# Optimization experiments

Hardware: AMD Instinct MI355X
Metric: run time of the kernel (lower is better)

## Reference

```python
import jax, jax.numpy as jnp
import numpy as np

B, S, V, H = 256, 1024, 256, 256


def setup_inputs() -> dict:
    key = jax.random.key(0)
    ks = jax.random.split(key, 12)
    s = 1.0 / np.sqrt(H)
    def u(k, shape):
        return jax.random.uniform(k, shape, jnp.float32, -s, s)
    return {
        "x": jax.random.normal(ks[0], (B, S, V), jnp.float32),
        "w_ih0": u(ks[1], (4 * H, V)),
        "w_hh0": u(ks[2], (4 * H, H)),
        "b_ih0": u(ks[3], (4 * H,)),
        "b_hh0": u(ks[4], (4 * H,)),
        "w_ih1": u(ks[5], (4 * H, H)),
        "w_hh1": u(ks[6], (4 * H, H)),
        "b_ih1": u(ks[7], (4 * H,)),
        "b_hh1": u(ks[8], (4 * H,)),
        "fc_w": u(ks[9], (V, H)),
        "fc_b": u(ks[10], (V,)),
    }


def _lstm_layer(inp, w_ih, w_hh, b_ih, b_hh):
    # inp: [B, S, D]. Precompute input contribution for all timesteps (big GEMM),
    # then scan the recurrence (PyTorch gate order: i, f, g, o).
    pre = jnp.einsum('bsd,gd->bsg', inp, w_ih) + b_ih + b_hh  # [B, S, 4H]
    h0 = jnp.zeros((inp.shape[0], w_hh.shape[1]), inp.dtype)
    c0 = jnp.zeros_like(h0)

    def step(carry, p):
        h, c = carry
        g = p + h @ w_hh.T  # [B, 4H]
        i, f, gg, o = jnp.split(g, 4, axis=-1)
        c = jax.nn.sigmoid(f) * c + jax.nn.sigmoid(i) * jnp.tanh(gg)
        h = jax.nn.sigmoid(o) * jnp.tanh(c)
        return (h, c), h

    _, hs = jax.lax.scan(step, (h0, c0), pre.transpose(1, 0, 2))  # hs: [S, B, H]
    return hs.transpose(1, 0, 2)


def reference(x, w_ih0, w_hh0, b_ih0, b_hh0, w_ih1, w_hh1, b_ih1, b_hh1, fc_w, fc_b):
    h1 = _lstm_layer(x, w_ih0, w_hh0, b_ih0, b_hh0)
    h2 = _lstm_layer(h1, w_ih1, w_hh1, b_ih1, b_hh1)
    logits = jnp.einsum('bsh,vh->bsv', h2, fc_w) + fc_b
    return jax.nn.log_softmax(logits, axis=-1)
```

## Files before the change

### kernel.cpp

```cpp
#include <hip/hip_runtime.h>
#include <cstdint>
#include <cstddef>


typedef __attribute__((ext_vector_type(8))) short bf16x8;
typedef __attribute__((ext_vector_type(4))) float f32x4;

#define DEVFN __device__ __forceinline__

constexpr unsigned SENT = 0xFFFFFFFFu;

DEVFN unsigned short f2bf(float f) {
  union { float f; unsigned u; } v; v.f = f;
  unsigned r = v.u + 0x7FFFu + ((v.u >> 16) & 1u);
  return (unsigned short)(r >> 16);
}
DEVFN float bf2f(unsigned short b) {
  union { unsigned u; float f; } v; v.u = ((unsigned)b) << 16;
  return v.f;
}
DEVFN int swz(int row, int colbyte) {
  return row * 512 + ((((colbyte >> 4) ^ (row & 7)) << 4) | (colbyte & 15));
}
DEVFN float sigm(float x) { return __builtin_amdgcn_rcpf(1.f + __expf(-x)); }
DEVFN float tanhfast(float x) {
  float ax = fabsf(x);
  float e  = __expf(-2.f * ax);
  float t  = (1.f - e) * __builtin_amdgcn_rcpf(1.f + e);
  return copysignf(t, x);
}

DEVFN unsigned aload(const unsigned* p) {
  return __hip_atomic_load(p, __ATOMIC_RELAXED, __HIP_MEMORY_SCOPE_AGENT);
}

DEVFN void spin16(unsigned hv[16], const unsigned* hs_tid) {
  while (true) {
    unsigned pend = 0;
#pragma unroll
    for (int k = 0; k < 16; ++k) pend |= (hv[k] == SENT) ? 1u : 0u;
    if (!pend) break;
#pragma unroll
    for (int k = 0; k < 16; ++k) hv[k] = aload(hs_tid + k * 128);
  }
}

__global__ void pack_w(const float* __restrict__ w, unsigned short* __restrict__ dst) {
  int bid = blockIdx.x;
  int lane = threadIdx.x;
  int col = (bid >> 3) * 16 + (lane & 15);
  int k0  = (bid & 7) * 32 + (lane >> 4) * 8;
  const float* src = w + (size_t)col * 256 + k0;
  unsigned short* d = dst + ((size_t)bid * 64 + lane) * 8;
#pragma unroll
  for (int j = 0; j < 8; ++j) d[j] = f2bf(src[j]);
}

__global__ __launch_bounds__(128, 1) void lstm_dual(
    const float* __restrict__ x,
    const unsigned short* __restrict__ Wih0, const unsigned short* __restrict__ Whh0,
    const float* __restrict__ bih0, const float* __restrict__ bhh0,
    const unsigned short* __restrict__ Wih1, const unsigned short* __restrict__ Whh1,
    const float* __restrict__ bih1, const float* __restrict__ bhh1,
    unsigned short* __restrict__ h1, unsigned short* __restrict__ h2)
{
  __shared__ char ldsA[8192];
  __shared__ char ldsB[8192];
  const int tid = threadIdx.x;
  const int w = tid >> 6, lane = tid & 63;
  const bool isL1 = blockIdx.x >= 128;
  const int b = isL1 ? (int)blockIdx.x - 128 : (int)blockIdx.x;
  const int m = b & 15, n = b >> 4;
  const int u16 = n * 2 + w;
  const int u   = u16 * 16 + (lane & 15);
  const int r0  = (lane >> 4) * 4;

  const unsigned short* Wih = isL1 ? Wih1 : Wih0;
  const unsigned short* Whh = isL1 ? Whh1 : Whh0;
  const float* bihp = isL1 ? bih1 : bih0;
  const float* bhhp = isL1 ? bhh1 : bhh0;
  unsigned short* hout = isL1 ? h2 : h1;

  bf16x8 bwih[4][8], bwhh[4][8];
#pragma unroll
  for (int g = 0; g < 4; ++g)
#pragma unroll
    for (int kt = 0; kt < 8; ++kt) {
      bwih[g][kt] = *(const bf16x8*)(Wih +
          ((((size_t)(g * 16 + u16)) * 8 + kt) * 64 + lane) * 8);
      bwhh[g][kt] = *(const bf16x8*)(Whh +
          ((((size_t)(g * 16 + u16)) * 8 + kt) * 64 + lane) * 8);
    }

  float bias[4];
#pragma unroll
  for (int g = 0; g < 4; ++g) bias[g] = bihp[g * 256 + u] + bhhp[g * 256 + u];

  float c[4] = {0.f, 0.f, 0.f, 0.f};

  if (!isL1) {
    const int xr = tid >> 3;
    const int xc = (tid & 7) * 32;
    float4 vv[8];
    {
      const float4* s = (const float4*)(x + ((size_t)(16 * m + xr) * 1024 + 0) * 256 + xc);
#pragma unroll
      for (int j = 0; j < 8; ++j) vv[j] = s[j];
    }

    for (int t = 0; t < 1024; ++t) {
#pragma unroll
      for (int s4 = 0; s4 < 4; ++s4) {
        uint4 o;
        o.x = f2bf(vv[2*s4].x)   | ((unsigned)f2bf(vv[2*s4].y)   << 16);
        o.y = f2bf(vv[2*s4].z)   | ((unsigned)f2bf(vv[2*s4].w)   << 16);
        o.z = f2bf(vv[2*s4+1].x) | ((unsigned)f2bf(vv[2*s4+1].y) << 16);
        o.w = f2bf(vv[2*s4+1].z) | ((unsigned)f2bf(vv[2*s4+1].w) << 16);
        *(uint4*)(&ldsB[swz(xr, xc * 2 + s4 * 16)]) = o;
      }
      if (t < 1023) {
        const float4* s = (const float4*)(x + ((size_t)(16 * m + xr) * 1024 + (t + 1)) * 256 + xc);
#pragma unroll
        for (int j = 0; j < 8; ++j) vv[j] = s[j];
      }
      unsigned hv[16];
      const unsigned* hs_tid = nullptr;
      if (t > 0) {
        hs_tid = (const unsigned*)h1 + ((size_t)(t - 1) * 256 + 16 * m) * 128 + tid;
#pragma unroll
        for (int k = 0; k < 16; ++k) hv[k] = aload(hs_tid + k * 128);
      }
      __syncthreads();

      f32x4 acc[4];
#pragma unroll
      for (int g = 0; g < 4; ++g) acc[g] = (f32x4){0.f, 0.f, 0.f, 0.f};
#pragma unroll
      for (int kt = 0; kt < 8; ++kt) {
        bf16x8 a = *(const bf16x8*)(&ldsB[swz(lane & 15, kt * 64 + (lane >> 4) * 16)]);
#pragma unroll
        for (int g = 0; g < 4; ++g)
          acc[g] = __builtin_amdgcn_mfma_f32_16x16x32_bf16(a, bwih[g][kt], acc[g], 0, 0, 0);
      }

      if (t > 0) {
        spin16(hv, hs_tid);
#pragma unroll
        for (int k = 0; k < 16; ++k)
          *(unsigned*)(&ldsA[swz(k, tid * 4)]) = hv[k];
        __syncthreads();
#pragma unroll
        for (int kt = 0; kt < 8; ++kt) {
          bf16x8 a = *(const bf16x8*)(&ldsA[swz(lane & 15, kt * 64 + (lane >> 4) * 16)]);
#pragma unroll
          for (int g = 0; g < 4; ++g)
            acc[g] = __builtin_amdgcn_mfma_f32_16x16x32_bf16(a, bwhh[g][kt], acc[g], 0, 0, 0);
        }
      } else {
        __syncthreads();
      }

      unsigned myh[4];
#pragma unroll
      for (int q = 0; q < 4; ++q) {
        float ia = acc[0][q] + bias[0];
        float fa = acc[1][q] + bias[1];
        float ga = acc[2][q] + bias[2];
        float oa = acc[3][q] + bias[3];
        c[q] = sigm(fa) * c[q] + sigm(ia) * tanhfast(ga);
        myh[q] = (unsigned)f2bf(sigm(oa) * tanhfast(c[q]));
      }
#pragma unroll
      for (int q = 0; q < 4; ++q) {
        unsigned ov = (unsigned)__shfl_xor((int)myh[q], 1, 64);
        if ((lane & 1) == 0) {
          unsigned word = (myh[q] & 0xFFFFu) | (ov << 16);
          unsigned* hp = (unsigned*)h1 + (((size_t)t * 256 + 16 * m + r0 + q) * 256 + u) / 2;
          __hip_atomic_store(hp, word, __ATOMIC_RELAXED, __HIP_MEMORY_SCOPE_AGENT);
        }
      }
    }
  } else {
    for (int t = 0; t < 1024; ++t) {
      unsigned hv1[16], hv2[16];
      const unsigned* hs1_tid = (const unsigned*)h1 + ((size_t)t * 256 + 16 * m) * 128 + tid;
      const unsigned* hs2_tid = nullptr;
#pragma unroll
      for (int k = 0; k < 16; ++k) hv1[k] = aload(hs1_tid + k * 128);
      if (t > 0) {
        hs2_tid = (const unsigned*)h2 + ((size_t)(t - 1) * 256 + 16 * m) * 128 + tid;
#pragma unroll
        for (int k = 0; k < 16; ++k) hv2[k] = aload(hs2_tid + k * 128);
      }

      spin16(hv1, hs1_tid);
#pragma unroll
      for (int k = 0; k < 16; ++k)
        *(unsigned*)(&ldsB[swz(k, tid * 4)]) = hv1[k];
      __syncthreads();

      f32x4 acc[4];
#pragma unroll
      for (int g = 0; g < 4; ++g) acc[g] = (f32x4){0.f, 0.f, 0.f, 0.f};
#pragma unroll
      for (int kt = 0; kt < 8; ++kt) {
        bf16x8 a = *(const bf16x8*)(&ldsB[swz(lane & 15, kt * 64 + (lane >> 4) * 16)]);
#pragma unroll
        for (int g = 0; g < 4; ++g)
          acc[g] = __builtin_amdgcn_mfma_f32_16x16x32_bf16(a, bwih[g][kt], acc[g], 0, 0, 0);
      }

      if (t > 0) {
        spin16(hv2, hs2_tid);
#pragma unroll
        for (int k = 0; k < 16; ++k)
          *(unsigned*)(&ldsA[swz(k, tid * 4)]) = hv2[k];
        __syncthreads();
#pragma unroll
        for (int kt = 0; kt < 8; ++kt) {
          bf16x8 a = *(const bf16x8*)(&ldsA[swz(lane & 15, kt * 64 + (lane >> 4) * 16)]);
#pragma unroll
          for (int g = 0; g < 4; ++g)
            acc[g] = __builtin_amdgcn_mfma_f32_16x16x32_bf16(a, bwhh[g][kt], acc[g], 0, 0, 0);
        }
      } else {
        __syncthreads();
      }

      unsigned myh[4];
#pragma unroll
      for (int q = 0; q < 4; ++q) {
        float ia = acc[0][q] + bias[0];
        float fa = acc[1][q] + bias[1];
        float ga = acc[2][q] + bias[2];
        float oa = acc[3][q] + bias[3];
        c[q] = sigm(fa) * c[q] + sigm(ia) * tanhfast(ga);
        myh[q] = (unsigned)f2bf(sigm(oa) * tanhfast(c[q]));
      }
#pragma unroll
      for (int q = 0; q < 4; ++q) {
        unsigned ov = (unsigned)__shfl_xor((int)myh[q], 1, 64);
        if ((lane & 1) == 0) {
          unsigned word = (myh[q] & 0xFFFFu) | (ov << 16);
          unsigned* hp = (unsigned*)h2 + (((size_t)t * 256 + 16 * m + r0 + q) * 256 + u) / 2;
          __hip_atomic_store(hp, word, __ATOMIC_RELAXED, __HIP_MEMORY_SCOPE_AGENT);
        }
      }
    }
  }
}

__global__ __launch_bounds__(256, 1) void fc_lsm(
    const unsigned short* __restrict__ h2,
    const unsigned short* __restrict__ Bp,
    const float* __restrict__ fcb,
    float* __restrict__ out)
{
  const int tid = threadIdx.x;
  const int wid = tid >> 6, lane = tid & 63;
  const int t = blockIdx.x >> 2, b0 = (blockIdx.x & 3) * 64;

  f32x4 acc[16];
#pragma unroll
  for (int nt = 0; nt < 16; ++nt) acc[nt] = (f32x4){0.f, 0.f, 0.f, 0.f};

#pragma unroll
  for (int kt = 0; kt < 8; ++kt) {
    bf16x8 a = *(const bf16x8*)(h2 +
        (((size_t)t * 256 + b0 + wid * 16 + (lane & 15)) * 256 +
         kt * 32 + (lane >> 4) * 8));
#pragma unroll
    for (int nt = 0; nt < 16; ++nt) {
      bf16x8 b = *(const bf16x8*)(Bp + (((size_t)nt * 8 + kt) * 64 + lane) * 8);
      acc[nt] = __builtin_amdgcn_mfma_f32_16x16x32_bf16(a, b, acc[nt], 0, 0, 0);
    }
  }
#pragma unroll
  for (int nt = 0; nt < 16; ++nt) {
    float bias = fcb[nt * 16 + (lane & 15)];
#pragma unroll
    for (int q = 0; q < 4; ++q) acc[nt][q] += bias;
  }

  float mx[4] = {-1e30f, -1e30f, -1e30f, -1e30f};
#pragma unroll
  for (int nt = 0; nt < 16; ++nt)
#pragma unroll
    for (int q = 0; q < 4; ++q) mx[q] = fmaxf(mx[q], acc[nt][q]);
#pragma unroll
  for (int d = 1; d < 16; d <<= 1)
#pragma unroll
    for (int q = 0; q < 4; ++q) mx[q] = fmaxf(mx[q], __shfl_xor(mx[q], d, 64));

  float sm[4] = {0.f, 0.f, 0.f, 0.f};
#pragma unroll
  for (int nt = 0; nt < 16; ++nt)
#pragma unroll
    for (int q = 0; q < 4; ++q) sm[q] += __expf(acc[nt][q] - mx[q]);
#pragma unroll
  for (int d = 1; d < 16; d <<= 1)
#pragma unroll
    for (int q = 0; q < 4; ++q) sm[q] += __shfl_xor(sm[q], d, 64);

  float lse[4];
#pragma unroll
  for (int q = 0; q < 4; ++q) lse[q] = mx[q] + __logf(sm[q]);

#pragma unroll
  for (int nt = 0; nt < 16; ++nt) {
#pragma unroll
    for (int q = 0; q < 4; ++q) {
      int b = b0 + wid * 16 + (lane >> 4) * 4 + q;
      out[((size_t)b * 1024 + t) * 256 + nt * 16 + (lane & 15)] = acc[nt][q] - lse[q];
    }
  }
}

__global__ void fill_marker(float* out, size_t nvals) {
  size_t i = (size_t)blockIdx.x * blockDim.x + threadIdx.x;
  if (i < nvals) out[i] = -7777.0f;
}

extern "C" void kernel_launch(void* const* d_in, const int* in_sizes, int n_in,
                              void* d_out, int out_size, void* d_ws, size_t ws_size,
                              hipStream_t stream)
{
  (void)in_sizes; (void)n_in;
  const float* x    = (const float*)d_in[0];
  const float* wih0 = (const float*)d_in[1];
  const float* whh0 = (const float*)d_in[2];
  const float* bih0 = (const float*)d_in[3];
  const float* bhh0 = (const float*)d_in[4];
  const float* wih1 = (const float*)d_in[5];
  const float* whh1 = (const float*)d_in[6];
  const float* bih1 = (const float*)d_in[7];
  const float* bhh1 = (const float*)d_in[8];
  const float* fcw  = (const float*)d_in[9];
  const float* fcb  = (const float*)d_in[10];
  float* out = (float*)d_out;

  const size_t o_wp0i = 0;
  const size_t o_wp0h = o_wp0i + 524288;
  const size_t o_wp1i = o_wp0h + 524288;
  const size_t o_wp1h = o_wp1i + 524288;
  const size_t o_fcp  = o_wp1h + 524288;
  const size_t o_h1   = o_fcp  + 131072;
  const size_t o_h2   = o_h1   + 134217728;
  const size_t need   = o_h2   + 134217728;

  if (ws_size < need) {
    size_t nv = (size_t)out_size;
    fill_marker<<<(unsigned)((nv + 1023) / 1024), 1024, 0, stream>>>(out, nv);
    return;
  }

  char* ws = (char*)d_ws;
  unsigned short* wp0i = (unsigned short*)(ws + o_wp0i);
  unsigned short* wp0h = (unsigned short*)(ws + o_wp0h);
  unsigned short* wp1i = (unsigned short*)(ws + o_wp1i);
  unsigned short* wp1h = (unsigned short*)(ws + o_wp1h);
  unsigned short* fcp  = (unsigned short*)(ws + o_fcp);
  unsigned short* h1   = (unsigned short*)(ws + o_h1);
  unsigned short* h2   = (unsigned short*)(ws + o_h2);

  pack_w<<<512, 64, 0, stream>>>(wih0, wp0i);
  pack_w<<<512, 64, 0, stream>>>(whh0, wp0h);
  pack_w<<<512, 64, 0, stream>>>(wih1, wp1i);
  pack_w<<<512, 64, 0, stream>>>(whh1, wp1h);
  pack_w<<<128, 64, 0, stream>>>(fcw,  fcp);

  hipMemsetAsync(h1, 0xFF, 134217728, stream);
  hipMemsetAsync(h2, 0xFF, 134217728, stream);

  lstm_dual<<<256, 128, 0, stream>>>(x, wp0i, wp0h, bih0, bhh0,
                                     wp1i, wp1h, bih1, bhh1, h1, h2);

  fc_lsm<<<4096, 256, 0, stream>>>(h2, fcp, fcb, out);
}
```

Baseline: 3.831 ms.

## Replace sentinel polling with per-wave progress flags between LSTM blocks

Hidden-state handoff between workgroups now uses per-wave counter flags, written after a vmcnt wait, instead of polling the data itself for a 0xFF sentinel. This drops the two 128MB sentinel memsets and lets consumers spin on a few flag words, then read h with 64-bit loads. Layer-1 blocks also reorder work so the recurrent h2 matmul runs before they wait on layer-0 output. The risk is ordering: relaxed atomics plus s_waitcnt must make the h stores visible before the flag store.

```diff
diff --git a/kernel.cpp b/kernel.cpp
--- a/kernel.cpp
+++ b/kernel.cpp
@@ -5,19 +5,14 @@
 
 typedef __attribute__((ext_vector_type(8))) short bf16x8;
 typedef __attribute__((ext_vector_type(4))) float f32x4;
+typedef unsigned long long ull;
 
 #define DEVFN __device__ __forceinline__
-
-constexpr unsigned SENT = 0xFFFFFFFFu;
 
 DEVFN unsigned short f2bf(float f) {
   union { float f; unsigned u; } v; v.f = f;
   unsigned r = v.u + 0x7FFFu + ((v.u >> 16) & 1u);
   return (unsigned short)(r >> 16);
-}
-DEVFN float bf2f(unsigned short b) {
-  union { unsigned u; float f; } v; v.u = ((unsigned)b) << 16;
-  return v.f;
 }
 DEVFN int swz(int row, int colbyte) {
   return row * 512 + ((((colbyte >> 4) ^ (row & 7)) << 4) | (colbyte & 15));
@@ -33,16 +28,15 @@
 DEVFN unsigned aload(const unsigned* p) {
   return __hip_atomic_load(p, __ATOMIC_RELAXED, __HIP_MEMORY_SCOPE_AGENT);
 }
-
-DEVFN void spin16(unsigned hv[16], const unsigned* hs_tid) {
-  while (true) {
-    unsigned pend = 0;
-#pragma unroll
-    for (int k = 0; k < 16; ++k) pend |= (hv[k] == SENT) ? 1u : 0u;
-    if (!pend) break;
-#pragma unroll
-    for (int k = 0; k < 16; ++k) hv[k] = aload(hs_tid + k * 128);
-  }
+DEVFN ull aload64(const ull* p) {
+  return __hip_atomic_load(p, __ATOMIC_RELAXED, __HIP_MEMORY_SCOPE_AGENT);
+}
+DEVFN void astore(unsigned* p, unsigned v) {
+  __hip_atomic_store(p, v, __ATOMIC_RELAXED, __HIP_MEMORY_SCOPE_AGENT);
+}
+
+DEVFN unsigned* flag_at(unsigned* f, int L, int m, int n, int w) {
+  return f + (((((L * 16 + m) * 8) + n) * 2 + w) << 4);
 }
 
 __global__ void pack_w(const float* __restrict__ w, unsigned short* __restrict__ dst) {
@@ -62,7 +56,8 @@
     const float* __restrict__ bih0, const float* __restrict__ bhh0,
     const unsigned short* __restrict__ Wih1, const unsigned short* __restrict__ Whh1,
     const float* __restrict__ bih1, const float* __restrict__ bhh1,
-    unsigned short* __restrict__ h1, unsigned short* __restrict__ h2)
+    unsigned short* __restrict__ h1, unsigned short* __restrict__ h2,
+    unsigned* __restrict__ flags)
 {
   __shared__ char ldsA[8192];
   __shared__ char ldsB[8192];
@@ -98,12 +93,18 @@
 
   float c[4] = {0.f, 0.f, 0.f, 0.f};
 
+  const int r = tid >> 3, cc = tid & 7;
+  const int Lown = isL1 ? 1 : 0;
+  unsigned* fown = flag_at(flags, Lown, m, n, w);
+  const unsigned* fh_0 = flag_at(flags, Lown, m, cc, 0);
+  const unsigned* fh_1 = flag_at(flags, Lown, m, cc, 1);
+  const unsigned* fs_0 = flag_at(flags, 0, m, cc, 0);
+  const unsigned* fs_1 = flag_at(flags, 0, m, cc, 1);
+
   if (!isL1) {
-    const int xr = tid >> 3;
-    const int xc = (tid & 7) * 32;
     float4 vv[8];
     {
-      const float4* s = (const float4*)(x + ((size_t)(16 * m + xr) * 1024 + 0) * 256 + xc);
+      const float4* s = (const float4*)(x + ((size_t)(16 * m + r) * 1024 + 0) * 256 + cc * 32);
 #pragma unroll
       for (int j = 0; j < 8; ++j) vv[j] = s[j];
     }
@@ -116,19 +117,12 @@
         o.y = f2bf(vv[2*s4].z)   | ((unsigned)f2bf(vv[2*s4].w)   << 16);
         o.z = f2bf(vv[2*s4+1].x) | ((unsigned)f2bf(vv[2*s4+1].y) << 16);
         o.w = f2bf(vv[2*s4+1].z) | ((unsigned)f2bf(vv[2*s4+1].w) << 16);
-        *(uint4*)(&ldsB[swz(xr, xc * 2 + s4 * 16)]) = o;
+        *(uint4*)(&ldsB[swz(r, cc * 64 + s4 * 16)]) = o;
       }
       if (t < 1023) {
-        const float4* s = (const float4*)(x + ((size_t)(16 * m + xr) * 1024 + (t + 1)) * 256 + xc);
+        const float4* s = (const float4*)(x + ((size_t)(16 * m + r) * 1024 + (t + 1)) * 256 + cc * 32);
 #pragma unroll
         for (int j = 0; j < 8; ++j) vv[j] = s[j];
-      }
-      unsigned hv[16];
-      const unsigned* hs_tid = nullptr;
-      if (t > 0) {
-        hs_tid = (const unsigned*)h1 + ((size_t)(t - 1) * 256 + 16 * m) * 128 + tid;
-#pragma unroll
-        for (int k = 0; k < 16; ++k) hv[k] = aload(hs_tid + k * 128);
       }
       __syncthreads();
 
@@ -144,11 +138,24 @@
       }
 
       if (t > 0) {
-        spin16(hv, hs_tid);
-#pragma unroll
-        for (int k = 0; k < 16; ++k)
-          *(unsigned*)(&ldsA[swz(k, tid * 4)]) = hv[k];
-        __syncthreads();
+        const unsigned tgt = (unsigned)t;
+        while (aload(fh_0) < tgt) {}
+        while (aload(fh_1) < tgt) {}
+        const ull* hs = (const ull*)h1 + ((size_t)(t - 1) * 256 + 16 * m + r) * 64 + cc * 8;
+        ull hv[8];
+#pragma unroll
+        for (int k = 0; k < 8; ++k) hv[k] = aload64(hs + k);
+#pragma unroll
+        for (int s4 = 0; s4 < 4; ++s4) {
+          uint4 o;
+          o.x = (unsigned)hv[2*s4];       o.y = (unsigned)(hv[2*s4] >> 32);
+          o.z = (unsigned)hv[2*s4+1];     o.w = (unsigned)(hv[2*s4+1] >> 32);
+          *(uint4*)(&ldsA[swz(r, cc * 64 + s4 * 16)]) = o;
+        }
+      }
+      __syncthreads();
+
+      if (t > 0) {
 #pragma unroll
         for (int kt = 0; kt < 8; ++kt) {
           bf16x8 a = *(const bf16x8*)(&ldsA[swz(lane & 15, kt * 64 + (lane >> 4) * 16)]);
@@ -156,8 +163,6 @@
           for (int g = 0; g < 4; ++g)
             acc[g] = __builtin_amdgcn_mfma_f32_16x16x32_bf16(a, bwhh[g][kt], acc[g], 0, 0, 0);
         }
-      } else {
-        __syncthreads();
       }
 
       unsigned myh[4];
@@ -176,55 +181,71 @@
         if ((lane & 1) == 0) {
           unsigned word = (myh[q] & 0xFFFFu) | (ov << 16);
           unsigned* hp = (unsigned*)h1 + (((size_t)t * 256 + 16 * m + r0 + q) * 256 + u) / 2;
-          __hip_atomic_store(hp, word, __ATOMIC_RELAXED, __HIP_MEMORY_SCOPE_AGENT);
-        }
-      }
+          astore(hp, word);
+        }
+      }
+      asm volatile("s_waitcnt vmcnt(0)" ::: "memory");
+      if (lane == 0) astore(fown, (unsigned)(t + 1));
     }
   } else {
     for (int t = 0; t < 1024; ++t) {
-      unsigned hv1[16], hv2[16];
-      const unsigned* hs1_tid = (const unsigned*)h1 + ((size_t)t * 256 + 16 * m) * 128 + tid;
-      const unsigned* hs2_tid = nullptr;
-#pragma unroll
-      for (int k = 0; k < 16; ++k) hv1[k] = aload(hs1_tid + k * 128);
+      ull hv2[8];
       if (t > 0) {
-        hs2_tid = (const unsigned*)h2 + ((size_t)(t - 1) * 256 + 16 * m) * 128 + tid;
-#pragma unroll
-        for (int k = 0; k < 16; ++k) hv2[k] = aload(hs2_tid + k * 128);
-      }
-
-      spin16(hv1, hs1_tid);
-#pragma unroll
-      for (int k = 0; k < 16; ++k)
-        *(unsigned*)(&ldsB[swz(k, tid * 4)]) = hv1[k];
+        const unsigned tgt = (unsigned)t;
+        while (aload(fh_0) < tgt) {}
+        while (aload(fh_1) < tgt) {}
+        const ull* hs2 = (const ull*)h2 + ((size_t)(t - 1) * 256 + 16 * m + r) * 64 + cc * 8;
+#pragma unroll
+        for (int k = 0; k < 8; ++k) hv2[k] = aload64(hs2 + k);
+      }
+      {
+        const unsigned tgt = (unsigned)(t + 1);
+        while (aload(fs_0) < tgt) {}
+        while (aload(fs_1) < tgt) {}
+      }
+      const ull* hs1 = (const ull*)h1 + ((size_t)t * 256 + 16 * m + r) * 64 + cc * 8;
+      ull hv1[8];
+#pragma unroll
+      for (int k = 0; k < 8; ++k) hv1[k] = aload64(hs1 + k);
+
+      if (t > 0) {
+#pragma unroll
+        for (int s4 = 0; s4 < 4; ++s4) {
+          uint4 o;
+          o.x = (unsigned)hv2[2*s4];      o.y = (unsigned)(hv2[2*s4] >> 32);
+          o.z = (unsigned)hv2[2*s4+1];    o.w = (unsigned)(hv2[2*s4+1] >> 32);
+          *(uint4*)(&ldsA[swz(r, cc * 64 + s4 * 16)]) = o;
+        }
+      }
       __syncthreads();
 
       f32x4 acc[4];
 #pragma unroll
       for (int g = 0; g < 4; ++g) acc[g] = (f32x4){0.f, 0.f, 0.f, 0.f};
+      if (t > 0) {
+#pragma unroll
+        for (int kt = 0; kt < 8; ++kt) {
+          bf16x8 a = *(const bf16x8*)(&ldsA[swz(lane & 15, kt * 64 + (lane >> 4) * 16)]);
+#pragma unroll
+          for (int g = 0; g < 4; ++g)
+            acc[g] = __builtin_amdgcn_mfma_f32_16x16x32_bf16(a, bwhh[g][kt], acc[g], 0, 0, 0);
+        }
+      }
+#pragma unroll
+      for (int s4 = 0; s4 < 4; ++s4) {
+        uint4 o;
+        o.x = (unsigned)hv1[2*s4];        o.y = (unsigned)(hv1[2*s4] >> 32);
+        o.z = (unsigned)hv1[2*s4+1];      o.w = (unsigned)(hv1[2*s4+1] >> 32);
+        *(uint4*)(&ldsB[swz(r, cc * 64 + s4 * 16)]) = o;
+      }
+      __syncthreads();
+
 #pragma unroll
       for (int kt = 0; kt < 8; ++kt) {
         bf16x8 a = *(const bf16x8*)(&ldsB[swz(lane & 15, kt * 64 + (lane >> 4) * 16)]);
 #pragma unroll
         for (int g = 0; g < 4; ++g)
           acc[g] = __builtin_amdgcn_mfma_f32_16x16x32_bf16(a, bwih[g][kt], acc[g], 0, 0, 0);
-      }
-
-      if (t > 0) {
-        spin16(hv2, hs2_tid);
-#pragma unroll
-        for (int k = 0; k < 16; ++k)
-          *(unsigned*)(&ldsA[swz(k, tid * 4)]) = hv2[k];
-        __syncthreads();
-#pragma unroll
-        for (int kt = 0; kt < 8; ++kt) {
-          bf16x8 a = *(const bf16x8*)(&ldsA[swz(lane & 15, kt * 64 + (lane >> 4) * 16)]);
-#pragma unroll
-          for (int g = 0; g < 4; ++g)
-            acc[g] = __builtin_amdgcn_mfma_f32_16x16x32_bf16(a, bwhh[g][kt], acc[g], 0, 0, 0);
-        }
-      } else {
-        __syncthreads();
       }
 
       unsigned myh[4];
@@ -243,9 +264,11 @@
         if ((lane & 1) == 0) {
           unsigned word = (myh[q] & 0xFFFFu) | (ov << 16);
           unsigned* hp = (unsigned*)h2 + (((size_t)t * 256 + 16 * m + r0 + q) * 256 + u) / 2;
-          __hip_atomic_store(hp, word, __ATOMIC_RELAXED, __HIP_MEMORY_SCOPE_AGENT);
-        }
-      }
+          astore(hp, word);
+        }
+      }
+      asm volatile("s_waitcnt vmcnt(0)" ::: "memory");
+      if (lane == 0) astore(fown, (unsigned)(t + 1));
     }
   }
 }
@@ -344,7 +367,8 @@
   const size_t o_wp1i = o_wp0h + 524288;
   const size_t o_wp1h = o_wp1i + 524288;
   const size_t o_fcp  = o_wp1h + 524288;
-  const size_t o_h1   = o_fcp  + 131072;
+  const size_t o_flg  = o_fcp  + 131072;
+  const size_t o_h1   = o_flg  + 32768;
   const size_t o_h2   = o_h1   + 134217728;
   const size_t need   = o_h2   + 134217728;
 
@@ -360,6 +384,7 @@
   unsigned short* wp1i = (unsigned short*)(ws + o_wp1i);
   unsigned short* wp1h = (unsigned short*)(ws + o_wp1h);
   unsigned short* fcp  = (unsigned short*)(ws + o_fcp);
+  unsigned*       flg  = (unsigned*)(ws + o_flg);
   unsigned short* h1   = (unsigned short*)(ws + o_h1);
   unsigned short* h2   = (unsigned short*)(ws + o_h2);
 
@@ -369,11 +394,10 @@
   pack_w<<<512, 64, 0, stream>>>(whh1, wp1h);
   pack_w<<<128, 64, 0, stream>>>(fcw,  fcp);
 
-  hipMemsetAsync(h1, 0xFF, 134217728, stream);
-  hipMemsetAsync(h2, 0xFF, 134217728, stream);
+  hipMemsetAsync(flg, 0, 32768, stream);
 
   lstm_dual<<<256, 128, 0, stream>>>(x, wp0i, wp0h, bih0, bhh0,
-                                     wp1i, wp1h, bih1, bhh1, h1, h2);
+                                     wp1i, wp1h, bih1, bhh1, h1, h2, flg);
 
   fc_lsm<<<4096, 256, 0, stream>>>(h2, fcp, fcb, out);
 }
```

Result: slower. 4.669 ms (+21.9%).

## Load MFMA A-fragments directly from global, dropping LDS staging and block barriers

Applied to the files above, without the earlier changes.

Each lane now loads its own MFMA A-operand fragment straight from global memory: the x rows with in-register bf16 conversion, and the hidden states through atomic loads. This removes the LDS round trip and both __syncthreads per timestep, so the two waves no longer synchronise with each other. In exchange, each lane issues 32 atomic loads and spins on them, twice the previous number, and both waves load the same h data redundantly. The x prefetch for the next timestep is also gone, so x load latency now sits on the critical path.

```diff
diff --git a/kernel.cpp b/kernel.cpp
--- a/kernel.cpp
+++ b/kernel.cpp
@@ -14,13 +14,6 @@
   union { float f; unsigned u; } v; v.f = f;
   unsigned r = v.u + 0x7FFFu + ((v.u >> 16) & 1u);
   return (unsigned short)(r >> 16);
-}
-DEVFN float bf2f(unsigned short b) {
-  union { unsigned u; float f; } v; v.u = ((unsigned)b) << 16;
-  return v.f;
-}
-DEVFN int swz(int row, int colbyte) {
-  return row * 512 + ((((colbyte >> 4) ^ (row & 7)) << 4) | (colbyte & 15));
 }
 DEVFN float sigm(float x) { return __builtin_amdgcn_rcpf(1.f + __expf(-x)); }
 DEVFN float tanhfast(float x) {
@@ -33,15 +26,25 @@
 DEVFN unsigned aload(const unsigned* p) {
   return __hip_atomic_load(p, __ATOMIC_RELAXED, __HIP_MEMORY_SCOPE_AGENT);
 }
-
-DEVFN void spin16(unsigned hv[16], const unsigned* hs_tid) {
+DEVFN void astore(unsigned* p, unsigned v) {
+  __hip_atomic_store(p, v, __ATOMIC_RELAXED, __HIP_MEMORY_SCOPE_AGENT);
+}
+
+DEVFN bf16x8 frag_of(unsigned d0, unsigned d1, unsigned d2, unsigned d3) {
+  union { uint4 u; bf16x8 v; } t;
+  t.u = make_uint4(d0, d1, d2, d3);
+  return t.v;
+}
+
+DEVFN void spin32(unsigned hv[32], const unsigned* base, int hi4) {
   while (true) {
     unsigned pend = 0;
 #pragma unroll
-    for (int k = 0; k < 16; ++k) pend |= (hv[k] == SENT) ? 1u : 0u;
+    for (int i = 0; i < 32; ++i) pend |= (hv[i] == SENT) ? 1u : 0u;
     if (!pend) break;
 #pragma unroll
-    for (int k = 0; k < 16; ++k) hv[k] = aload(hs_tid + k * 128);
+    for (int i = 0; i < 32; ++i)
+      hv[i] = aload(base + (i >> 2) * 16 + hi4 + (i & 3));
   }
 }
 
@@ -64,22 +67,21 @@
     const float* __restrict__ bih1, const float* __restrict__ bhh1,
     unsigned short* __restrict__ h1, unsigned short* __restrict__ h2)
 {
-  __shared__ char ldsA[8192];
-  __shared__ char ldsB[8192];
   const int tid = threadIdx.x;
   const int w = tid >> 6, lane = tid & 63;
   const bool isL1 = blockIdx.x >= 128;
-  const int b = isL1 ? (int)blockIdx.x - 128 : (int)blockIdx.x;
+  const int b = (int)blockIdx.x & 127;
   const int m = b & 15, n = b >> 4;
   const int u16 = n * 2 + w;
   const int u   = u16 * 16 + (lane & 15);
   const int r0  = (lane >> 4) * 4;
+  const int row = lane & 15;
+  const int hi4 = (lane >> 4) * 4;
 
   const unsigned short* Wih = isL1 ? Wih1 : Wih0;
   const unsigned short* Whh = isL1 ? Whh1 : Whh0;
   const float* bihp = isL1 ? bih1 : bih0;
   const float* bhhp = isL1 ? bhh1 : bhh0;
-  unsigned short* hout = isL1 ? h2 : h1;
 
   bf16x8 bwih[4][8], bwhh[4][8];
 #pragma unroll
@@ -99,65 +101,50 @@
   float c[4] = {0.f, 0.f, 0.f, 0.f};
 
   if (!isL1) {
-    const int xr = tid >> 3;
-    const int xc = (tid & 7) * 32;
-    float4 vv[8];
-    {
-      const float4* s = (const float4*)(x + ((size_t)(16 * m + xr) * 1024 + 0) * 256 + xc);
-#pragma unroll
-      for (int j = 0; j < 8; ++j) vv[j] = s[j];
-    }
-
     for (int t = 0; t < 1024; ++t) {
-#pragma unroll
-      for (int s4 = 0; s4 < 4; ++s4) {
-        uint4 o;
-        o.x = f2bf(vv[2*s4].x)   | ((unsigned)f2bf(vv[2*s4].y)   << 16);
-        o.y = f2bf(vv[2*s4].z)   | ((unsigned)f2bf(vv[2*s4].w)   << 16);
-        o.z = f2bf(vv[2*s4+1].x) | ((unsigned)f2bf(vv[2*s4+1].y) << 16);
-        o.w = f2bf(vv[2*s4+1].z) | ((unsigned)f2bf(vv[2*s4+1].w) << 16);
-        *(uint4*)(&ldsB[swz(xr, xc * 2 + s4 * 16)]) = o;
-      }
-      if (t < 1023) {
-        const float4* s = (const float4*)(x + ((size_t)(16 * m + xr) * 1024 + (t + 1)) * 256 + xc);
-#pragma unroll
-        for (int j = 0; j < 8; ++j) vv[j] = s[j];
-      }
-      unsigned hv[16];
-      const unsigned* hs_tid = nullptr;
+      unsigned hv[32];
+      const unsigned* hb = nullptr;
       if (t > 0) {
-        hs_tid = (const unsigned*)h1 + ((size_t)(t - 1) * 256 + 16 * m) * 128 + tid;
-#pragma unroll
-        for (int k = 0; k < 16; ++k) hv[k] = aload(hs_tid + k * 128);
-      }
-      __syncthreads();
+        hb = (const unsigned*)h1 + ((size_t)(t - 1) * 256 + 16 * m + row) * 128;
+#pragma unroll
+        for (int i = 0; i < 32; ++i)
+          hv[i] = aload(hb + (i >> 2) * 16 + hi4 + (i & 3));
+      }
+
+      bf16x8 xa[8];
+      {
+        const float* xb = x + ((size_t)(16 * m + row) * 1024 + (size_t)t) * 256 + (hi4 * 2);
+#pragma unroll
+        for (int kt = 0; kt < 8; ++kt) {
+          float4 f0 = *(const float4*)(xb + kt * 32);
+          float4 f1 = *(const float4*)(xb + kt * 32 + 4);
+          unsigned d0 = f2bf(f0.x) | ((unsigned)f2bf(f0.y) << 16);
+          unsigned d1 = f2bf(f0.z) | ((unsigned)f2bf(f0.w) << 16);
+          unsigned d2 = f2bf(f1.x) | ((unsigned)f2bf(f1.y) << 16);
+          unsigned d3 = f2bf(f1.z) | ((unsigned)f2bf(f1.w) << 16);
+          xa[kt] = frag_of(d0, d1, d2, d3);
+        }
+      }
 
       f32x4 acc[4];
 #pragma unroll
       for (int g = 0; g < 4; ++g) acc[g] = (f32x4){0.f, 0.f, 0.f, 0.f};
 #pragma unroll
       for (int kt = 0; kt < 8; ++kt) {
-        bf16x8 a = *(const bf16x8*)(&ldsB[swz(lane & 15, kt * 64 + (lane >> 4) * 16)]);
 #pragma unroll
         for (int g = 0; g < 4; ++g)
-          acc[g] = __builtin_amdgcn_mfma_f32_16x16x32_bf16(a, bwih[g][kt], acc[g], 0, 0, 0);
+          acc[g] = __builtin_amdgcn_mfma_f32_16x16x32_bf16(xa[kt], bwih[g][kt], acc[g], 0, 0, 0);
       }
 
       if (t > 0) {
-        spin16(hv, hs_tid);
-#pragma unroll
-        for (int k = 0; k < 16; ++k)
-          *(unsigned*)(&ldsA[swz(k, tid * 4)]) = hv[k];
-        __syncthreads();
+        spin32(hv, hb, hi4);
 #pragma unroll
         for (int kt = 0; kt < 8; ++kt) {
-          bf16x8 a = *(const bf16x8*)(&ldsA[swz(lane & 15, kt * 64 + (lane >> 4) * 16)]);
+          bf16x8 a = frag_of(hv[kt*4], hv[kt*4+1], hv[kt*4+2], hv[kt*4+3]);
 #pragma unroll
           for (int g = 0; g < 4; ++g)
             acc[g] = __builtin_amdgcn_mfma_f32_16x16x32_bf16(a, bwhh[g][kt], acc[g], 0, 0, 0);
         }
-      } else {
-        __syncthreads();
       }
 
       unsigned myh[4];
@@ -176,55 +163,47 @@
         if ((lane & 1) == 0) {
           unsigned word = (myh[q] & 0xFFFFu) | (ov << 16);
           unsigned* hp = (unsigned*)h1 + (((size_t)t * 256 + 16 * m + r0 + q) * 256 + u) / 2;
-          __hip_atomic_store(hp, word, __ATOMIC_RELAXED, __HIP_MEMORY_SCOPE_AGENT);
+          astore(hp, word);
         }
       }
     }
   } else {
     for (int t = 0; t < 1024; ++t) {
-      unsigned hv1[16], hv2[16];
-      const unsigned* hs1_tid = (const unsigned*)h1 + ((size_t)t * 256 + 16 * m) * 128 + tid;
-      const unsigned* hs2_tid = nullptr;
-#pragma unroll
-      for (int k = 0; k < 16; ++k) hv1[k] = aload(hs1_tid + k * 128);
+      unsigned hv2[32], hv1[32];
+      const unsigned* b2 = nullptr;
       if (t > 0) {
-        hs2_tid = (const unsigned*)h2 + ((size_t)(t - 1) * 256 + 16 * m) * 128 + tid;
-#pragma unroll
-        for (int k = 0; k < 16; ++k) hv2[k] = aload(hs2_tid + k * 128);
-      }
-
-      spin16(hv1, hs1_tid);
-#pragma unroll
-      for (int k = 0; k < 16; ++k)
-        *(unsigned*)(&ldsB[swz(k, tid * 4)]) = hv1[k];
-      __syncthreads();
+        b2 = (const unsigned*)h2 + ((size_t)(t - 1) * 256 + 16 * m + row) * 128;
+#pragma unroll
+        for (int i = 0; i < 32; ++i)
+          hv2[i] = aload(b2 + (i >> 2) * 16 + hi4 + (i & 3));
+      }
+      const unsigned* b1 = (const unsigned*)h1 + ((size_t)t * 256 + 16 * m + row) * 128;
+#pragma unroll
+      for (int i = 0; i < 32; ++i)
+        hv1[i] = aload(b1 + (i >> 2) * 16 + hi4 + (i & 3));
+
+      spin32(hv1, b1, hi4);
 
       f32x4 acc[4];
 #pragma unroll
       for (int g = 0; g < 4; ++g) acc[g] = (f32x4){0.f, 0.f, 0.f, 0.f};
 #pragma unroll
       for (int kt = 0; kt < 8; ++kt) {
-        bf16x8 a = *(const bf16x8*)(&ldsB[swz(lane & 15, kt * 64 + (lane >> 4) * 16)]);
+        bf16x8 a = frag_of(hv1[kt*4], hv1[kt*4+1], hv1[kt*4+2], hv1[kt*4+3]);
 #pragma unroll
         for (int g = 0; g < 4; ++g)
           acc[g] = __builtin_amdgcn_mfma_f32_16x16x32_bf16(a, bwih[g][kt], acc[g], 0, 0, 0);
       }
 
       if (t > 0) {
-        spin16(hv2, hs2_tid);
-#pragma unroll
-        for (int k = 0; k < 16; ++k)
-          *(unsigned*)(&ldsA[swz(k, tid * 4)]) = hv2[k];
-        __syncthreads();
+        spin32(hv2, b2, hi4);
 #pragma unroll
         for (int kt = 0; kt < 8; ++kt) {
-          bf16x8 a = *(const bf16x8*)(&ldsA[swz(lane & 15, kt * 64 + (lane >> 4) * 16)]);
+          bf16x8 a = frag_of(hv2[kt*4], hv2[kt*4+1], hv2[kt*4+2], hv2[kt*4+3]);
 #pragma unroll
           for (int g = 0; g < 4; ++g)
             acc[g] = __builtin_amdgcn_mfma_f32_16x16x32_bf16(a, bwhh[g][kt], acc[g], 0, 0, 0);
         }
-      } else {
-        __syncthreads();
       }
 
       unsigned myh[4];
@@ -243,7 +222,7 @@
         if ((lane & 1) == 0) {
           unsigned word = (myh[q] & 0xFFFFu) | (ov << 16);
           unsigned* hp = (unsigned*)h2 + (((size_t)t * 256 + 16 * m + r0 + q) * 256 + u) / 2;
-          __hip_atomic_store(hp, word, __ATOMIC_RELAXED, __HIP_MEMORY_SCOPE_AGENT);
+          astore(hp, word);
         }
       }
     }
```

Result: slower. 10.86 ms (+183.6%).
